# Kernel optimization log

Measured on AMD Instinct MI355X. Metric: run time of the kernel, lower is better.

The kernel has to match this reference:

```python
import jax, jax.numpy as jnp
import numpy as np

NUM_HEADS = 12
SIZE_PER_HEAD = 64
NEG_INF = -10000.0


def setup_inputs() -> dict:
    key = jax.random.key(0)
    k1, k2, k3, k4 = jax.random.split(key, 4)
    B, S, D = 2, 2048, 768
    x = jax.random.normal(k1, (B, S, D), dtype=jnp.float32)
    mask = jax.random.randint(k2, (B, S, S), 0, 2, dtype=jnp.int32)
    std = 0.02
    Wq = jax.random.normal(k3, (D, NUM_HEADS * SIZE_PER_HEAD), dtype=jnp.float32) * std
    Wk = jax.random.normal(k4, (D, NUM_HEADS * SIZE_PER_HEAD), dtype=jnp.float32) * std
    bq = jnp.zeros((NUM_HEADS * SIZE_PER_HEAD,), dtype=jnp.float32)
    bk = jnp.zeros((NUM_HEADS * SIZE_PER_HEAD,), dtype=jnp.float32)
    return {"x": x, "mask": mask, "Wq": Wq, "bq": bq, "Wk": Wk, "bk": bk}


def reference(x, mask, Wq, bq, Wk, bk):
    B, S, D = x.shape
    H, dh = NUM_HEADS, SIZE_PER_HEAD
    # Dense query/key projections (no activation), then split heads: [B,H,S,dh]
    q = (x @ Wq + bq).reshape(B, S, H, dh).transpose(0, 2, 1, 3)
    k = (x @ Wk + bk).reshape(B, S, H, dh).transpose(0, 2, 1, 3)
    # Scaled dot-product scores: [B,H,S,S]
    scores = jnp.einsum("bhqd,bhkd->bhqk", q, k) / jnp.sqrt(jnp.float32(dh))
    # Mask: [B,S,S] -> [B,1,S,S]; zeros get large negative additive bias
    adder = (1.0 - mask.astype(jnp.float32))[:, None, :, :] * NEG_INF
    probs = jax.nn.softmax(scores + adder, axis=-1)
    # dropout is identity at inference (training=None)
    return probs
```

## Files before the change

### kernel.cpp

```cpp
#include <hip/hip_runtime.h>
#include <stdint.h>

#define NUM_HEADS 12
#define DH 64
#define SEQ 2048
#define BATCH 2
#define DM 768
#define NQK 1536
#define LOG2E 1.44269504088896340736f

typedef short short8 __attribute__((ext_vector_type(8)));
typedef short short4_t __attribute__((ext_vector_type(4)));
typedef float f32x4 __attribute__((ext_vector_type(4)));

__device__ __forceinline__ short bf16_rne(float f) {
    union { float f; uint32_t u; } v; v.f = f;
    return (short)((v.u + 0x7FFFu + ((v.u >> 16) & 1u)) >> 16);
}

__global__ __launch_bounds__(256) void prep_kernel(const float* __restrict__ Wq,
                                                   const float* __restrict__ Wk,
                                                   const float* __restrict__ x,
                                                   const int* __restrict__ mask,
                                                   short* __restrict__ Wt,
                                                   short* __restrict__ Xb,
                                                   unsigned long long* __restrict__ Mb) {
    __shared__ float tile[32][33];
    const int bid = blockIdx.x;
    const int t = threadIdx.x;
    if (bid < 1152) {
        int n0 = (bid % 48) * 32;
        int k0 = (bid / 48) * 32;
        int tx = t & 31;
        int ty = t >> 5;
        const float* src = (n0 < DM) ? Wq : Wk;
        int nn0 = (n0 < DM) ? n0 : n0 - DM;
#pragma unroll
        for (int j = 0; j < 4; ++j) {
            int k = ty + 8 * j;
            tile[k][tx] = src[(size_t)(k0 + k) * DM + nn0 + tx];
        }
        __syncthreads();
#pragma unroll
        for (int j = 0; j < 4; ++j) {
            int n = ty + 8 * j;
            Wt[(size_t)(n0 + n) * DM + k0 + tx] = bf16_rne(tile[tx][n]);
        }
    } else if (bid < 1920) {
        size_t base = (size_t)(bid - 1152) * 4096;
#pragma unroll
        for (int j = 0; j < 4; ++j) {
            size_t i = base + (size_t)(t + j * 256) * 4;
            f32x4 v = *(const f32x4*)(x + i);
            short4_t s;
#pragma unroll
            for (int e = 0; e < 4; ++e) s[e] = bf16_rne(v[e]);
            *(short4_t*)(Xb + i) = s;
        }
    } else {
        int wid = (bid - 1920) * 4 + (t >> 6);
        int lane = t & 63;
        size_t base = (size_t)wid * 8;
#pragma unroll
        for (int i = 0; i < 8; ++i) {
            size_t w = base + i;
            int v = mask[w * 64 + lane];
            unsigned long long bal = __ballot(v != 0);
            if (lane == 0) Mb[w] = bal;
        }
    }
}

__global__ __launch_bounds__(256) void proj_kernel(const short* __restrict__ Xb,
                                                   const short* __restrict__ Wt,
                                                   const float* __restrict__ bq,
                                                   const float* __restrict__ bk,
                                                   short* __restrict__ QK) {
    __shared__ short As[128 * 72];
    __shared__ short Bs[128 * 72];
    const int m0 = blockIdx.x * 128;
    const int n0 = blockIdx.y * 128;
    const int t = threadIdx.x;
    const int lane = t & 63;
    const int w = t >> 6;
    const int wr = w >> 1, wc = w & 1;
    const int lr = lane & 15;
    const int lk = lane >> 4;

    f32x4 acc[4][4] = {};

    for (int k0 = 0; k0 < DM; k0 += 64) {
#pragma unroll
        for (int j = 0; j < 4; ++j) {
            int idx = t + 256 * j;
            int row = idx >> 3;
            int ch = idx & 7;
            *(short8*)&As[row * 72 + ch * 8] =
                *(const short8*)&Xb[(size_t)(m0 + row) * DM + k0 + ch * 8];
            *(short8*)&Bs[row * 72 + ch * 8] =
                *(const short8*)&Wt[(size_t)(n0 + row) * DM + k0 + ch * 8];
        }
        __syncthreads();
#pragma unroll
        for (int kk = 0; kk < 2; ++kk) {
            short8 a[4], bfr[4];
#pragma unroll
            for (int m = 0; m < 4; ++m)
                a[m] = *(short8*)&As[(wr * 64 + m * 16 + lr) * 72 + kk * 32 + lk * 8];
#pragma unroll
            for (int n = 0; n < 4; ++n)
                bfr[n] = *(short8*)&Bs[(wc * 64 + n * 16 + lr) * 72 + kk * 32 + lk * 8];
#pragma unroll
            for (int m = 0; m < 4; ++m)
#pragma unroll
                for (int n = 0; n < 4; ++n)
                    acc[m][n] = __builtin_amdgcn_mfma_f32_16x16x32_bf16(a[m], bfr[n], acc[m][n], 0, 0, 0);
        }
        __syncthreads();
    }

    const int orow = m0 + wr * 64;
    const int ocol = n0 + wc * 64;
#pragma unroll
    for (int m = 0; m < 4; ++m) {
#pragma unroll
        for (int n = 0; n < 4; ++n) {
            int col = ocol + n * 16 + lr;
            float bias = (col < DM) ? bq[col] : bk[col - DM];
            float scale = (col < DM) ? 0.125f * LOG2E : 1.0f;
#pragma unroll
            for (int r = 0; r < 4; ++r) {
                int row = orow + m * 16 + lk * 4 + r;
                QK[(size_t)row * NQK + col] = bf16_rne((acc[m][n][r] + bias) * scale);
            }
        }
    }
}

__global__ __launch_bounds__(256) void attn_kernel(const short* __restrict__ QK,
                                                   const unsigned long long* __restrict__ Mb,
                                                   float* __restrict__ out) {
    __shared__ short Ks[2][64 * 72];
    const int qblk = blockIdx.x;
    const int h = blockIdx.y;
    const int b = blockIdx.z;
    const int t = threadIdx.x;
    const int lane = t & 63;
    const int w = t >> 6;
    const int lr = lane & 15;
    const int lk = lane >> 4;
    const int wq = qblk * 64 + w * 16;

    short8 aq[2];
#pragma unroll
    for (int ks = 0; ks < 2; ++ks)
        aq[ks] = *(const short8*)&QK[(size_t)(b * SEQ + wq + lr) * NQK + h * DH + ks * 32 + lk * 8];

    float lrow[4] = {0.f, 0.f, 0.f, 0.f};
    const size_t mrow0 = (size_t)b * SEQ * (SEQ / 64);
    const int srow = t >> 3, sch = t & 7;

#define ATT_STAGE(KT)                                                                             \
    {                                                                                             \
        _Pragma("unroll") for (int tb = 0; tb < 2; ++tb) {                                        \
            *(short8*)&Ks[tb][srow * 72 + sch * 8] =                                              \
                *(const short8*)&QK[(size_t)(b * SEQ + (KT) + tb * 64 + srow) * NQK + DM +        \
                                    h * DH + sch * 8];                                            \
            *(short8*)&Ks[tb][(srow + 32) * 72 + sch * 8] =                                       \
                *(const short8*)&QK[(size_t)(b * SEQ + (KT) + tb * 64 + srow + 32) * NQK + DM +   \
                                    h * DH + sch * 8];                                            \
        }                                                                                         \
    }

    for (int kt = 0; kt < SEQ; kt += 128) {
        ATT_STAGE(kt)
        __syncthreads();
#pragma unroll
        for (int tb = 0; tb < 2; ++tb) {
            f32x4 sc[4];
#pragma unroll
            for (int nf = 0; nf < 4; ++nf) {
                short8 k0 = *(short8*)&Ks[tb][(nf * 16 + lr) * 72 + lk * 8];
                short8 k1 = *(short8*)&Ks[tb][(nf * 16 + lr) * 72 + 32 + lk * 8];
                f32x4 a = {0.f, 0.f, 0.f, 0.f};
                a = __builtin_amdgcn_mfma_f32_16x16x32_bf16(aq[0], k0, a, 0, 0, 0);
                a = __builtin_amdgcn_mfma_f32_16x16x32_bf16(aq[1], k1, a, 0, 0, 0);
                sc[nf] = a;
            }
#pragma unroll
            for (int r = 0; r < 4; ++r) {
                int q = wq + lk * 4 + r;
                unsigned long long mbs = Mb[mrow0 + (size_t)q * 32 + ((kt >> 6) + tb)] >> lr;
                float s = 0.f;
#pragma unroll
                for (int nf = 0; nf < 4; ++nf) {
                    float e = __builtin_amdgcn_exp2f(sc[nf][r]);
                    s += ((mbs >> (nf * 16)) & 1ull) ? e : 0.f;
                }
                lrow[r] += s;
            }
        }
        __syncthreads();
    }

    float inv[4];
#pragma unroll
    for (int r = 0; r < 4; ++r) {
        float l = lrow[r];
        l += __shfl_xor(l, 1, 64);
        l += __shfl_xor(l, 2, 64);
        l += __shfl_xor(l, 4, 64);
        l += __shfl_xor(l, 8, 64);
        inv[r] = 1.0f / l;
    }

    for (int kt = 0; kt < SEQ; kt += 128) {
        ATT_STAGE(kt)
        __syncthreads();
#pragma unroll
        for (int tb = 0; tb < 2; ++tb) {
            f32x4 sc[4];
#pragma unroll
            for (int nf = 0; nf < 4; ++nf) {
                short8 k0 = *(short8*)&Ks[tb][(nf * 16 + lr) * 72 + lk * 8];
                short8 k1 = *(short8*)&Ks[tb][(nf * 16 + lr) * 72 + 32 + lk * 8];
                f32x4 a = {0.f, 0.f, 0.f, 0.f};
                a = __builtin_amdgcn_mfma_f32_16x16x32_bf16(aq[0], k0, a, 0, 0, 0);
                a = __builtin_amdgcn_mfma_f32_16x16x32_bf16(aq[1], k1, a, 0, 0, 0);
                sc[nf] = a;
            }
#pragma unroll
            for (int r = 0; r < 4; ++r) {
                int q = wq + lk * 4 + r;
                unsigned long long mbs = Mb[mrow0 + (size_t)q * 32 + ((kt >> 6) + tb)] >> lr;
                float* op = &out[((size_t)((b * NUM_HEADS + h) * SEQ + q)) * SEQ + kt + tb * 64 + lr];
#pragma unroll
                for (int nf = 0; nf < 4; ++nf) {
                    float p = __builtin_amdgcn_exp2f(sc[nf][r]) * inv[r];
                    op[nf * 16] = ((mbs >> (nf * 16)) & 1ull) ? p : 0.f;
                }
            }
        }
        __syncthreads();
    }
#undef ATT_STAGE
}

extern "C" void kernel_launch(void* const* d_in, const int* in_sizes, int n_in,
                              void* d_out, int out_size, void* d_ws, size_t ws_size,
                              hipStream_t stream) {
    (void)in_sizes; (void)n_in; (void)out_size; (void)ws_size;
    const float* x = (const float*)d_in[0];
    const int* mask = (const int*)d_in[1];
    const float* Wq = (const float*)d_in[2];
    const float* bq = (const float*)d_in[3];
    const float* Wk = (const float*)d_in[4];
    const float* bk = (const float*)d_in[5];
    float* out = (float*)d_out;

    short* Wt = (short*)d_ws;
    short* Xb = Wt + (size_t)NQK * DM;
    short* QK = Xb + (size_t)BATCH * SEQ * DM;
    unsigned long long* Mb =
        (unsigned long long*)(QK + (size_t)BATCH * SEQ * NQK);

    prep_kernel<<<dim3(6016), 256, 0, stream>>>(Wq, Wk, x, mask, Wt, Xb, Mb);
    proj_kernel<<<dim3(BATCH * SEQ / 128, NQK / 128), 256, 0, stream>>>(Xb, Wt, bq, bk, QK);
    attn_kernel<<<dim3(SEQ / 64, NUM_HEADS, BATCH), 256, 0, stream>>>(QK, Mb, out);
}
```

Before: 171.7 us.

## Keep masked exponentials in registers to skip second score pass

The attention kernel now has each block handle 16 query rows across all 2048 keys. The four waves split the key columns, and the masked exp values (128 floats per lane) stay in registers, so the scores are no longer recomputed in a second pass. The MFMA operands are swapped so each lane holds 4 consecutive key columns. This allows vectorized float4 output stores and a single mask word load per tile. It costs heavy register pressure, a cross-wave shared reduction, and 4x more blocks that each reload all of K.

```diff
diff --git a/kernel.cpp b/kernel.cpp
--- a/kernel.cpp
+++ b/kernel.cpp
@@ -137,10 +137,11 @@
     }
 }
 
-__global__ __launch_bounds__(256) void attn_kernel(const short* __restrict__ QK,
-                                                   const unsigned long long* __restrict__ Mb,
-                                                   float* __restrict__ out) {
-    __shared__ short Ks[2][64 * 72];
+__global__ __launch_bounds__(256, 2) void attn_kernel(const short* __restrict__ QK,
+                                                      const unsigned long long* __restrict__ Mb,
+                                                      float* __restrict__ out) {
+    __shared__ short Ks[256 * 72];
+    __shared__ float red[4][16];
     const int qblk = blockIdx.x;
     const int h = blockIdx.y;
     const int b = blockIdx.z;
@@ -149,101 +150,64 @@
     const int w = t >> 6;
     const int lr = lane & 15;
     const int lk = lane >> 4;
-    const int wq = qblk * 64 + w * 16;
-
-    short8 aq[2];
-#pragma unroll
-    for (int ks = 0; ks < 2; ++ks)
-        aq[ks] = *(const short8*)&QK[(size_t)(b * SEQ + wq + lr) * NQK + h * DH + ks * 32 + lk * 8];
-
-    float lrow[4] = {0.f, 0.f, 0.f, 0.f};
-    const size_t mrow0 = (size_t)b * SEQ * (SEQ / 64);
-    const int srow = t >> 3, sch = t & 7;
-
-#define ATT_STAGE(KT)                                                                             \
-    {                                                                                             \
-        _Pragma("unroll") for (int tb = 0; tb < 2; ++tb) {                                        \
-            *(short8*)&Ks[tb][srow * 72 + sch * 8] =                                              \
-                *(const short8*)&QK[(size_t)(b * SEQ + (KT) + tb * 64 + srow) * NQK + DM +        \
-                                    h * DH + sch * 8];                                            \
-            *(short8*)&Ks[tb][(srow + 32) * 72 + sch * 8] =                                       \
-                *(const short8*)&QK[(size_t)(b * SEQ + (KT) + tb * 64 + srow + 32) * NQK + DM +   \
-                                    h * DH + sch * 8];                                            \
-        }                                                                                         \
-    }
-
-    for (int kt = 0; kt < SEQ; kt += 128) {
-        ATT_STAGE(kt)
-        __syncthreads();
-#pragma unroll
-        for (int tb = 0; tb < 2; ++tb) {
-            f32x4 sc[4];
-#pragma unroll
-            for (int nf = 0; nf < 4; ++nf) {
-                short8 k0 = *(short8*)&Ks[tb][(nf * 16 + lr) * 72 + lk * 8];
-                short8 k1 = *(short8*)&Ks[tb][(nf * 16 + lr) * 72 + 32 + lk * 8];
-                f32x4 a = {0.f, 0.f, 0.f, 0.f};
-                a = __builtin_amdgcn_mfma_f32_16x16x32_bf16(aq[0], k0, a, 0, 0, 0);
-                a = __builtin_amdgcn_mfma_f32_16x16x32_bf16(aq[1], k1, a, 0, 0, 0);
-                sc[nf] = a;
+    const int q = qblk * 16 + lr;
+
+    const short8 aq0 = *(const short8*)&QK[(size_t)(b * SEQ + q) * NQK + h * DH + lk * 8];
+    const short8 aq1 = *(const short8*)&QK[(size_t)(b * SEQ + q) * NQK + h * DH + 32 + lk * 8];
+
+    const size_t mrow = (size_t)b * SEQ * (SEQ / 64) + (size_t)q * 32;
+    const int sch = t & 7;
+
+    f32x4 e[8][4];
+    float lsum = 0.0f;
+
+#pragma unroll
+    for (int it = 0; it < 8; ++it) {
+        const int kt0 = it * 256;
+#pragma unroll
+        for (int j = 0; j < 8; ++j) {
+            int row = (t >> 3) + 32 * j;
+            *(short8*)&Ks[row * 72 + sch * 8] =
+                *(const short8*)&QK[(size_t)(b * SEQ + kt0 + row) * NQK + DM + h * DH + sch * 8];
+        }
+        __syncthreads();
+        const unsigned long long mbs = Mb[mrow + it * 4 + w] >> (lk * 4);
+#pragma unroll
+        for (int nf = 0; nf < 4; ++nf) {
+            short8 k0 = *(short8*)&Ks[(w * 64 + nf * 16 + lr) * 72 + lk * 8];
+            short8 k1 = *(short8*)&Ks[(w * 64 + nf * 16 + lr) * 72 + 32 + lk * 8];
+            f32x4 a = {0.f, 0.f, 0.f, 0.f};
+            a = __builtin_amdgcn_mfma_f32_16x16x32_bf16(k0, aq0, a, 0, 0, 0);
+            a = __builtin_amdgcn_mfma_f32_16x16x32_bf16(k1, aq1, a, 0, 0, 0);
+            f32x4 ev;
+#pragma unroll
+            for (int r = 0; r < 4; ++r) {
+                float ex = __builtin_amdgcn_exp2f(a[r]);
+                ev[r] = ((mbs >> (nf * 16 + r)) & 1ull) ? ex : 0.f;
+                lsum += ev[r];
             }
-#pragma unroll
-            for (int r = 0; r < 4; ++r) {
-                int q = wq + lk * 4 + r;
-                unsigned long long mbs = Mb[mrow0 + (size_t)q * 32 + ((kt >> 6) + tb)] >> lr;
-                float s = 0.f;
-#pragma unroll
-                for (int nf = 0; nf < 4; ++nf) {
-                    float e = __builtin_amdgcn_exp2f(sc[nf][r]);
-                    s += ((mbs >> (nf * 16)) & 1ull) ? e : 0.f;
-                }
-                lrow[r] += s;
-            }
-        }
-        __syncthreads();
-    }
-
-    float inv[4];
-#pragma unroll
-    for (int r = 0; r < 4; ++r) {
-        float l = lrow[r];
-        l += __shfl_xor(l, 1, 64);
-        l += __shfl_xor(l, 2, 64);
-        l += __shfl_xor(l, 4, 64);
-        l += __shfl_xor(l, 8, 64);
-        inv[r] = 1.0f / l;
-    }
-
-    for (int kt = 0; kt < SEQ; kt += 128) {
-        ATT_STAGE(kt)
-        __syncthreads();
-#pragma unroll
-        for (int tb = 0; tb < 2; ++tb) {
-            f32x4 sc[4];
-#pragma unroll
-            for (int nf = 0; nf < 4; ++nf) {
-                short8 k0 = *(short8*)&Ks[tb][(nf * 16 + lr) * 72 + lk * 8];
-                short8 k1 = *(short8*)&Ks[tb][(nf * 16 + lr) * 72 + 32 + lk * 8];
-                f32x4 a = {0.f, 0.f, 0.f, 0.f};
-                a = __builtin_amdgcn_mfma_f32_16x16x32_bf16(aq[0], k0, a, 0, 0, 0);
-                a = __builtin_amdgcn_mfma_f32_16x16x32_bf16(aq[1], k1, a, 0, 0, 0);
-                sc[nf] = a;
-            }
-#pragma unroll
-            for (int r = 0; r < 4; ++r) {
-                int q = wq + lk * 4 + r;
-                unsigned long long mbs = Mb[mrow0 + (size_t)q * 32 + ((kt >> 6) + tb)] >> lr;
-                float* op = &out[((size_t)((b * NUM_HEADS + h) * SEQ + q)) * SEQ + kt + tb * 64 + lr];
-#pragma unroll
-                for (int nf = 0; nf < 4; ++nf) {
-                    float p = __builtin_amdgcn_exp2f(sc[nf][r]) * inv[r];
-                    op[nf * 16] = ((mbs >> (nf * 16)) & 1ull) ? p : 0.f;
-                }
-            }
-        }
-        __syncthreads();
-    }
-#undef ATT_STAGE
+            e[it][nf] = ev;
+        }
+        __syncthreads();
+    }
+
+    lsum += __shfl_xor(lsum, 16, 64);
+    lsum += __shfl_xor(lsum, 32, 64);
+    if (lane < 16) red[w][lr] = lsum;
+    __syncthreads();
+    const float inv = 1.0f / (red[0][lr] + red[1][lr] + red[2][lr] + red[3][lr]);
+
+    const size_t orow = ((size_t)((b * NUM_HEADS + h) * SEQ) + q) * SEQ;
+#pragma unroll
+    for (int it = 0; it < 8; ++it) {
+#pragma unroll
+        for (int nf = 0; nf < 4; ++nf) {
+            f32x4 p;
+#pragma unroll
+            for (int r = 0; r < 4; ++r) p[r] = e[it][nf][r] * inv;
+            *(f32x4*)&out[orow + it * 256 + w * 64 + nf * 16 + lk * 4] = p;
+        }
+    }
 }
 
 extern "C" void kernel_launch(void* const* d_in, const int* in_sizes, int n_in,
@@ -266,5 +230,5 @@
 
     prep_kernel<<<dim3(6016), 256, 0, stream>>>(Wq, Wk, x, mask, Wt, Xb, Mb);
     proj_kernel<<<dim3(BATCH * SEQ / 128, NQK / 128), 256, 0, stream>>>(Xb, Wt, bq, bk, QK);
-    attn_kernel<<<dim3(SEQ / 64, NUM_HEADS, BATCH), 256, 0, stream>>>(QK, Mb, out);
-}
+    attn_kernel<<<dim3(SEQ / 16, NUM_HEADS, BATCH), 256, 0, stream>>>(QK, Mb, out);
+}
```

Result: slower. 194.3 us (+13.1%).
